# Kernel optimization log

Measured on AMD Instinct MI355X. Metric: run time of the kernel, lower is better.

## Reference

```python
import jax, jax.numpy as jnp
import numpy as np

B, T, C, H = 8, 4096, 384, 64

def setup_inputs() -> dict:
    key = jax.random.key(0)
    k1, k2, k3, k4 = jax.random.split(key, 4)
    x = jax.random.normal(k1, (B, T, C), dtype=jnp.float32)
    Wq = jax.random.normal(k2, (C, H), dtype=jnp.float32) / np.sqrt(C)
    Wk = jax.random.normal(k3, (C, H), dtype=jnp.float32) / np.sqrt(C)
    Wv = jax.random.normal(k4, (C, H), dtype=jnp.float32) / np.sqrt(C)
    return {"x": x, "Wq": Wq, "Wk": Wk, "Wv": Wv}

def reference(x, Wq, Wk, Wv):
    # single-head causal self-attention (dropout in eval mode = identity)
    T_ = x.shape[1]
    q = jnp.einsum('btc,ch->bth', x, Wq)   # [B,T,H]
    k = jnp.einsum('btc,ch->bth', x, Wk)   # [B,T,H]
    v = jnp.einsum('btc,ch->bth', x, Wv)   # [B,T,H]
    scale = 1.0 / jnp.sqrt(jnp.float32(Wq.shape[1]))
    wei = jnp.einsum('bth,bsh->bts', q, k) * scale        # [B,T,T]
    causal = jnp.tril(jnp.ones((T_, T_), dtype=bool))
    wei = jnp.where(causal, wei, -jnp.inf)
    wei = jax.nn.softmax(wei, axis=-1)
    out = jnp.einsum('bts,bsh->bth', wei, v)              # [B,T,H]
    return out
```

## Files before the change

### kernel.cpp

```cpp
#include <hip/hip_runtime.h>
#include <hip/hip_bf16.h>
#include <cstdint>
#include <cstddef>

#define BATCH 8
#define SEQ   4096
#define CDIM  384
#define HDIM  64
#define NSPL  8

typedef __attribute__((ext_vector_type(8)))  __bf16 bf16x8;
typedef __attribute__((ext_vector_type(4)))  float  f32x4;
typedef __attribute__((ext_vector_type(16))) float  f32x16;
typedef __attribute__((ext_vector_type(4)))  short  short4v;

#if __has_builtin(__builtin_amdgcn_permlane32_swap)
#define HAVE_PERMLANE 1
#else
#define HAVE_PERMLANE 0
#endif

typedef __attribute__((address_space(3))) char lds_char;
typedef const __attribute__((address_space(1))) char gbl_char;

static __device__ __forceinline__ void gl_lds16(const void* g, void* l) {
  __builtin_amdgcn_global_load_lds((gbl_char*)g, (lds_char*)l, 16, 0, 0);
}

static __device__ __forceinline__ short f2bf(float f) {
  union { float f; uint32_t u; } v; v.f = f;
  uint32_t r = v.u + 0x7fffu + ((v.u >> 16) & 1u);
  return (short)(r >> 16);
}

static __device__ __forceinline__ float bf2f(short s) {
  union { uint32_t u; float f; } t;
  t.u = ((uint32_t)(uint16_t)s) << 16;
  return t.f;
}

static __device__ __forceinline__ uint32_t cvtpk(float lo, float hi) {
  uint32_t r;
  asm("v_cvt_pk_bf16_f32 %0, %1, %2" : "=v"(r) : "v"(lo), "v"(hi));
  return r;
}

static __device__ __forceinline__ float fexp2(float x) {
  float r;
  asm("v_exp_f32 %0, %1" : "=v"(r) : "v"(x));
  return r;
}

static __device__ __forceinline__ f32x4 mfma16(bf16x8 a, bf16x8 b, f32x4 c) {
  return __builtin_amdgcn_mfma_f32_16x16x32_bf16(a, b, c, 0, 0, 0);
}

static __device__ __forceinline__ f32x16 mfma32(bf16x8 a, bf16x8 b, f32x16 c) {
  return __builtin_amdgcn_mfma_f32_32x32x16_bf16(a, b, c, 0, 0, 0);
}

static __device__ __forceinline__ f32x4 zero4() {
  f32x4 z = {0.f, 0.f, 0.f, 0.f};
  return z;
}

static __device__ __forceinline__ float xhalf(float x, int hi) {
#if HAVE_PERMLANE
  union { float f; uint32_t u; } a; a.f = x;
  auto r = __builtin_amdgcn_permlane32_swap(a.u, a.u, false, false);
  union { uint32_t u; float f; } o; o.u = hi ? r[0] : r[1];
  return o.f;
#else
  return __shfl_xor(x, 32, 64);
#endif
}

static __device__ __forceinline__ void swap32(uint32_t& a, uint32_t& b, int hi) {
#if HAVE_PERMLANE
  auto r = __builtin_amdgcn_permlane32_swap(a, b, false, false);
  a = r[0]; b = r[1];
#else
  uint32_t sa = (uint32_t)__shfl_xor((int)a, 32, 64);
  uint32_t sb = (uint32_t)__shfl_xor((int)b, 32, 64);
  uint32_t na = hi ? sb : a;
  uint32_t nb = hi ? b : sa;
  a = na; b = nb;
#endif
}

static __device__ __forceinline__ float tmax16(const f32x16& v) {
  float a = fmaxf(fmaxf(v[0], v[1]), v[2]);
  float b = fmaxf(fmaxf(v[3], v[4]), v[5]);
  float c = fmaxf(fmaxf(v[6], v[7]), v[8]);
  float d = fmaxf(fmaxf(v[9], v[10]), v[11]);
  float e = fmaxf(fmaxf(v[12], v[13]), v[14]);
  float f = fmaxf(fmaxf(a, b), c);
  float g = fmaxf(fmaxf(d, e), v[15]);
  return fmaxf(f, g);
}

__global__ __launch_bounds__(256) void wpack_kernel(
    const float* __restrict__ Wq, const float* __restrict__ Wk,
    const float* __restrict__ Wv, short* __restrict__ Wt) {
  int idx = blockIdx.x * 256 + threadIdx.x;
  if (idx >= 192 * CDIM) return;
  int n = idx / CDIM;
  int c = idx - n * CDIM;
  int m = n >> 6, h = n & 63;
  const float* W = (m == 0) ? Wq : (m == 1) ? Wk : Wv;
  float s = (m == 0) ? 0.18033688011112042f : 1.0f;
  Wt[idx] = f2bf(W[c * HDIM + h] * s);
}

#define KPAD 136

__global__ __launch_bounds__(256) void qkv_kernel(
    const float* __restrict__ x, const short* __restrict__ Wt,
    short* __restrict__ qb, short* __restrict__ kb, short* __restrict__ vT) {
  __shared__ short xs[2][64][KPAD];
  const int tid = threadIdx.x;
  const int tokbase = blockIdx.x * 64;
  const float4* xg = (const float4*)(x + (size_t)tokbase * CDIM);

  for (int i = tid; i < 2048; i += 256) {
    int r = i >> 5, c4 = i & 31;
    float4 v = xg[r * 96 + c4];
    uint2 st; st.x = cvtpk(v.x, v.y); st.y = cvtpk(v.z, v.w);
    *(uint2*)&xs[0][r][c4 * 4] = st;
  }
  __syncthreads();

  const int wave = tid >> 6;
  const int lane = tid & 63;
  const int l16  = lane & 15;
  const int lq   = lane >> 4;

  f32x4 acc[4][3];
  #pragma unroll
  for (int ai = 0; ai < 4; ++ai)
    #pragma unroll
    for (int j = 0; j < 3; ++j) acc[ai][j] = zero4();

  for (int ch = 0; ch < 3; ++ch) {
    if (ch < 2) {
      const int nb = (ch + 1) & 1;
      for (int i = tid; i < 2048; i += 256) {
        int r = i >> 5, c4 = i & 31;
        float4 v = xg[r * 96 + (ch + 1) * 32 + c4];
        uint2 st; st.x = cvtpk(v.x, v.y); st.y = cvtpk(v.z, v.w);
        *(uint2*)&xs[nb][r][c4 * 4] = st;
      }
    }
    const int cb = ch & 1;
    #pragma unroll
    for (int kk = 0; kk < 4; ++kk) {
      const int k0 = kk * 32;
      bf16x8 a[4];
      #pragma unroll
      for (int ai = 0; ai < 4; ++ai)
        a[ai] = *(const bf16x8*)&xs[cb][ai * 16 + l16][k0 + lq * 8];
      bf16x8 bb[3];
      #pragma unroll
      for (int j = 0; j < 3; ++j) {
        const int nt = wave * 3 + j;
        bb[j] = *(const bf16x8*)&Wt[(size_t)(nt * 16 + l16) * CDIM +
                                    ch * 128 + k0 + lq * 8];
      }
      #pragma unroll
      for (int ai = 0; ai < 4; ++ai)
        #pragma unroll
        for (int j = 0; j < 3; ++j)
          acc[ai][j] = mfma16(a[ai], bb[j], acc[ai][j]);
    }
    __syncthreads();
  }

  const int b     = tokbase >> 12;
  const int tloc0 = tokbase & (SEQ - 1);
  #pragma unroll
  for (int j = 0; j < 3; ++j) {
    const int col = (wave * 3 + j) * 16 + l16;
    const int mat = col >> 6;
    const int h   = col & 63;
    #pragma unroll
    for (int ai = 0; ai < 4; ++ai) {
      const int row0 = ai * 16 + lq * 4;
      if (mat < 2) {
        short* dst = mat ? kb : qb;
        #pragma unroll
        for (int r = 0; r < 4; ++r)
          dst[(size_t)(tokbase + row0 + r) * HDIM + h] = f2bf(acc[ai][j][r]);
      } else {
        union { uint32_t u[2]; short4v s; } sv;
        sv.u[0] = cvtpk(acc[ai][j][0], acc[ai][j][1]);
        sv.u[1] = cvtpk(acc[ai][j][2], acc[ai][j][3]);
        *(short4v*)&vT[(size_t)(b * HDIM + h) * SEQ + (tloc0 + row0)] = sv.s;
      }
    }
  }
}

__global__ __launch_bounds__(256, 3) void attn_kernel(
    const short* __restrict__ qb, const short* __restrict__ kb,
    const short* __restrict__ vT, short* __restrict__ opart,
    float2* __restrict__ mlw) {
  __shared__ short kvbuf[2][2][4096];

  const int tid  = threadIdx.x;
  const int wave = tid >> 6;
  const int lane = tid & 63;
  const int l31  = lane & 31;
  const int hi   = lane >> 5;
  const int bid  = blockIdx.x;
  const int b    = bid & 7;
  const int idx  = bid >> 3;
  const int qt   = 31 - (idx >> 3);
  const int part = idx & 7;
  const int nkv  = 2 * qt + 2;
  const int base = nkv >> 3;
  const int rem  = nkv & 7;
  const int scnt = base + (part < rem ? 1 : 0);
  const int sbeg = part * base + (part < rem ? part : rem);
  const int q0   = qt << 7;
  const int qw0  = q0 + wave * 32;
  const size_t bT = (size_t)b * SEQ;

  const char* kg = (const char*)(kb + bT * HDIM);
  const char* vg = (const char*)(vT + (size_t)b * HDIM * SEQ);

  const int rsub = lane >> 3;
  const int gcol = ((lane & 7) << 4) ^ (rsub << 4);
  const int krb  = wave * 16;

  f32x16 oacc[2];
  #pragma unroll
  for (int hb = 0; hb < 2; ++hb)
    #pragma unroll
    for (int r = 0; r < 16; ++r) oacc[hb][r] = 0.f;
  float m = -1e30f, l = 0.f;

  if (scnt > 0) {
    bf16x8 qf[4];
    {
      const short* qrow = qb + (bT + qw0 + l31) * HDIM + hi * 8;
      #pragma unroll
      for (int t = 0; t < 4; ++t)
        qf[t] = *(const bf16x8*)(qrow + 16 * t);
    }
    const int sw = (l31 & 7) << 4;
    int colk[4];
    #pragma unroll
    for (int t = 0; t < 4; ++t) colk[t] = ((t * 32) + hi * 16) ^ sw;
    const int rbase = l31 * 128;

    {
      const int sf = sbeg << 6;
      #pragma unroll
      for (int i = 0; i < 2; ++i) {
        const int r = krb + i * 8;
        gl_lds16(kg + (size_t)(sf + r + rsub) * 128 + gcol,
                 (char*)&kvbuf[0][0][0] + r * 128);
        gl_lds16(vg + (size_t)(r + rsub) * 8192 + (size_t)sf * 2 + gcol,
                 (char*)&kvbuf[0][1][0] + r * 128);
      }
    }
    __syncthreads();

    int cur = 0;
    for (int it = 0; it < scnt; ++it) {
      const int s0 = (sbeg + it) << 6;
      if (it + 1 < scnt) {
        const int s1 = s0 + 64;
        const int nb = cur ^ 1;
        #pragma unroll
        for (int i = 0; i < 2; ++i) {
          const int r = krb + i * 8;
          gl_lds16(kg + (size_t)(s1 + r + rsub) * 128 + gcol,
                   (char*)&kvbuf[nb][0][0] + r * 128);
          gl_lds16(vg + (size_t)(r + rsub) * 8192 + (size_t)s1 * 2 + gcol,
                   (char*)&kvbuf[nb][1][0] + r * 128);
        }
      }

      if (s0 <= qw0 + 31) {
        const char* bufc = (const char*)kvbuf + cur * 16384;

        f32x16 sacc[2];
        #pragma unroll
        for (int sb = 0; sb < 2; ++sb) {
          #pragma unroll
          for (int r = 0; r < 16; ++r) sacc[sb][r] = 0.f;
          #pragma unroll
          for (int t = 0; t < 4; ++t) {
            bf16x8 kf = *(const bf16x8*)(bufc + sb * 4096 + rbase + colk[t]);
            sacc[sb] = mfma32(kf, qf[t], sacc[sb]);
          }
        }

        if (s0 + 63 > qw0) {
          const int qg = qw0 + l31;
          #pragma unroll
          for (int sb = 0; sb < 2; ++sb)
            #pragma unroll
            for (int r = 0; r < 16; ++r) {
              const int sg = s0 + sb * 32 + (r & 3) + 8 * (r >> 2) + 4 * hi;
              if (sg > qg) sacc[sb][r] = -3e38f;
            }
        }

        float pm = fmaxf(tmax16(sacc[0]), tmax16(sacc[1]));
        pm = fmaxf(pm, xhalf(pm, hi));

        if (!__all(pm <= m + 8.f)) {
          const float mn = fmaxf(m, pm);
          const float sc = fexp2(m - mn);
          m = mn; l *= sc;
          #pragma unroll
          for (int hb = 0; hb < 2; ++hb)
            #pragma unroll
            for (int r = 0; r < 16; ++r) oacc[hb][r] *= sc;
        }

        float p[2][16];
        #pragma unroll
        for (int sb = 0; sb < 2; ++sb)
          #pragma unroll
          for (int r = 0; r < 16; ++r)
            p[sb][r] = fexp2(sacc[sb][r] - m);
        float t8[8];
        #pragma unroll
        for (int sb = 0; sb < 2; ++sb)
          #pragma unroll
          for (int g = 0; g < 4; ++g)
            t8[sb * 4 + g] = (p[sb][4 * g] + p[sb][4 * g + 1]) +
                             (p[sb][4 * g + 2] + p[sb][4 * g + 3]);
        float rs = ((t8[0] + t8[1]) + (t8[2] + t8[3])) +
                   ((t8[4] + t8[5]) + (t8[6] + t8[7]));
        rs += xhalf(rs, hi);
        l += rs;

        uint32_t w[2][4][2];
        #pragma unroll
        for (int sb = 0; sb < 2; ++sb)
          #pragma unroll
          for (int g = 0; g < 4; ++g) {
            w[sb][g][0] = cvtpk(p[sb][4 * g + 0], p[sb][4 * g + 1]);
            w[sb][g][1] = cvtpk(p[sb][4 * g + 2], p[sb][4 * g + 3]);
          }

        bf16x8 pf[4];
        #pragma unroll
        for (int sb = 0; sb < 2; ++sb)
          #pragma unroll
          for (int t = 0; t < 2; ++t) {
            uint32_t a0 = w[sb][2 * t][0], b0 = w[sb][2 * t + 1][0];
            uint32_t a1 = w[sb][2 * t][1], b1 = w[sb][2 * t + 1][1];
            swap32(a0, b0, hi);
            swap32(a1, b1, hi);
            union { uint32_t u[4]; bf16x8 v; } uu;
            uu.u[0] = a0; uu.u[1] = a1; uu.u[2] = b0; uu.u[3] = b1;
            pf[sb * 2 + t] = uu.v;
          }

        __builtin_amdgcn_s_setprio(1);
        #pragma unroll
        for (int hb = 0; hb < 2; ++hb)
          #pragma unroll
          for (int ks = 0; ks < 4; ++ks) {
            bf16x8 vf = *(const bf16x8*)(bufc + 8192 + hb * 4096 + rbase + colk[ks]);
            oacc[hb] = mfma32(vf, pf[ks], oacc[hb]);
          }
        __builtin_amdgcn_s_setprio(0);
      }

      __syncthreads();
      cur ^= 1;
    }
  }

  short* obase = opart + (size_t)part * ((size_t)BATCH * SEQ * HDIM);
  const int q = qw0 + l31;
  #pragma unroll
  for (int hb = 0; hb < 2; ++hb)
    #pragma unroll
    for (int g = 0; g < 4; ++g) {
      uint2 st;
      st.x = cvtpk(oacc[hb][4 * g + 0], oacc[hb][4 * g + 1]);
      st.y = cvtpk(oacc[hb][4 * g + 2], oacc[hb][4 * g + 3]);
      *(uint2*)&obase[(bT + q) * HDIM + hb * 32 + 8 * g + 4 * hi] = st;
    }
  if (lane < 32) {
    float2 ml; ml.x = m; ml.y = l;
    mlw[part * (BATCH * SEQ) + bT + q] = ml;
  }
}

__global__ __launch_bounds__(256) void merge_kernel(
    float* __restrict__ out, const short* __restrict__ opart,
    const float2* __restrict__ mlw) {
  const int g   = blockIdx.x * 256 + threadIdx.x;
  const int row = g >> 4;
  const int c4  = (g & 15) << 2;
  float2 ml[NSPL];
  float mm = -3.4e38f;
  #pragma unroll
  for (int i = 0; i < NSPL; ++i) {
    ml[i] = mlw[i * (BATCH * SEQ) + row];
    mm = fmaxf(mm, ml[i].x);
  }
  float w[NSPL];
  float ls = 0.f;
  #pragma unroll
  for (int i = 0; i < NSPL; ++i) {
    w[i] = fexp2(ml[i].x - mm);
    ls += w[i] * ml[i].y;
  }
  const size_t stride = (size_t)BATCH * SEQ * HDIM;
  const size_t off = (size_t)row * HDIM + c4;
  float a0 = 0.f, a1 = 0.f, a2 = 0.f, a3 = 0.f;
  #pragma unroll
  for (int i = 0; i < NSPL; ++i) {
    short4v s = *(const short4v*)&opart[i * stride + off];
    a0 += w[i] * bf2f(s[0]);
    a1 += w[i] * bf2f(s[1]);
    a2 += w[i] * bf2f(s[2]);
    a3 += w[i] * bf2f(s[3]);
  }
  const float inv = 1.0f / ls;
  float4 r;
  r.x = a0 * inv; r.y = a1 * inv; r.z = a2 * inv; r.w = a3 * inv;
  *(float4*)&out[off] = r;
}

extern "C" void kernel_launch(void* const* d_in, const int* in_sizes, int n_in,
                              void* d_out, int out_size, void* d_ws, size_t ws_size,
                              hipStream_t stream) {
  (void)in_sizes; (void)n_in; (void)out_size; (void)ws_size;
  const float* x  = (const float*)d_in[0];
  const float* Wq = (const float*)d_in[1];
  const float* Wk = (const float*)d_in[2];
  const float* Wv = (const float*)d_in[3];

  const size_t qkvb = (size_t)BATCH * SEQ * HDIM * sizeof(short);
  const size_t opb  = (size_t)NSPL * BATCH * SEQ * HDIM * sizeof(short);
  const size_t mlb  = (size_t)NSPL * BATCH * SEQ * sizeof(float2);
  char* ws = (char*)d_ws;
  short*  qb    = (short*)(ws);
  short*  kb    = (short*)(ws + qkvb);
  short*  vT    = (short*)(ws + 2 * qkvb);
  short*  opart = (short*)(ws + 3 * qkvb);
  float2* mlw   = (float2*)(ws + 3 * qkvb + opb);
  short*  Wt    = (short*)(ws + 3 * qkvb + opb + mlb);

  wpack_kernel<<<dim3((192 * CDIM + 255) / 256), dim3(256), 0, stream>>>(Wq, Wk, Wv, Wt);
  qkv_kernel<<<dim3(BATCH * SEQ / 64), dim3(256), 0, stream>>>(x, Wt, qb, kb, vT);
  attn_kernel<<<dim3(2048), dim3(256), 0, stream>>>(qb, kb, vT, opart, mlw);
  merge_kernel<<<dim3(BATCH * SEQ * HDIM / 4 / 256), dim3(256), 0, stream>>>(
      (float*)d_out, opart, mlw);
}
```

Before: 69.87 us.

## Enlarge attention query tile to 256 rows with 8-wave blocks

Each attention block now uses 512 threads (8 waves) covering a 256-row query tile instead of 128, and the grid is halved. Every K/V tile loaded into LDS is therefore shared by twice as many query rows, which cuts global-to-LDS traffic per query, and each wave issues one load per matrix instead of two. The row-sum cross-half reduction also moves out of the loop to a single exchange at the end. In exchange, blocks are larger and fewer, which can hurt load balance across the causal triangle, and occupancy is capped at 2 blocks per CU.

```diff
diff --git a/kernel.cpp b/kernel.cpp
--- a/kernel.cpp
+++ b/kernel.cpp
@@ -200,7 +200,7 @@
   }
 }
 
-__global__ __launch_bounds__(256, 3) void attn_kernel(
+__global__ __launch_bounds__(512, 2) void attn_kernel(
     const short* __restrict__ qb, const short* __restrict__ kb,
     const short* __restrict__ vT, short* __restrict__ opart,
     float2* __restrict__ mlw) {
@@ -214,14 +214,14 @@
   const int bid  = blockIdx.x;
   const int b    = bid & 7;
   const int idx  = bid >> 3;
-  const int qt   = 31 - (idx >> 3);
+  const int qt   = 15 - (idx >> 3);
   const int part = idx & 7;
-  const int nkv  = 2 * qt + 2;
+  const int nkv  = 4 * qt + 4;
   const int base = nkv >> 3;
   const int rem  = nkv & 7;
   const int scnt = base + (part < rem ? 1 : 0);
   const int sbeg = part * base + (part < rem ? part : rem);
-  const int q0   = qt << 7;
+  const int q0   = qt << 8;
   const int qw0  = q0 + wave * 32;
   const size_t bT = (size_t)b * SEQ;
 
@@ -230,7 +230,7 @@
 
   const int rsub = lane >> 3;
   const int gcol = ((lane & 7) << 4) ^ (rsub << 4);
-  const int krb  = wave * 16;
+  const int krb  = wave * 8;
 
   f32x16 oacc[2];
   #pragma unroll
@@ -255,14 +255,10 @@
 
     {
       const int sf = sbeg << 6;
-      #pragma unroll
-      for (int i = 0; i < 2; ++i) {
-        const int r = krb + i * 8;
-        gl_lds16(kg + (size_t)(sf + r + rsub) * 128 + gcol,
-                 (char*)&kvbuf[0][0][0] + r * 128);
-        gl_lds16(vg + (size_t)(r + rsub) * 8192 + (size_t)sf * 2 + gcol,
-                 (char*)&kvbuf[0][1][0] + r * 128);
-      }
+      gl_lds16(kg + (size_t)(sf + krb + rsub) * 128 + gcol,
+               (char*)&kvbuf[0][0][0] + krb * 128);
+      gl_lds16(vg + (size_t)(krb + rsub) * 8192 + (size_t)sf * 2 + gcol,
+               (char*)&kvbuf[0][1][0] + krb * 128);
     }
     __syncthreads();
 
@@ -272,14 +268,10 @@
       if (it + 1 < scnt) {
         const int s1 = s0 + 64;
         const int nb = cur ^ 1;
-        #pragma unroll
-        for (int i = 0; i < 2; ++i) {
-          const int r = krb + i * 8;
-          gl_lds16(kg + (size_t)(s1 + r + rsub) * 128 + gcol,
-                   (char*)&kvbuf[nb][0][0] + r * 128);
-          gl_lds16(vg + (size_t)(r + rsub) * 8192 + (size_t)s1 * 2 + gcol,
-                   (char*)&kvbuf[nb][1][0] + r * 128);
-        }
+        gl_lds16(kg + (size_t)(s1 + krb + rsub) * 128 + gcol,
+                 (char*)&kvbuf[nb][0][0] + krb * 128);
+        gl_lds16(vg + (size_t)(krb + rsub) * 8192 + (size_t)s1 * 2 + gcol,
+                 (char*)&kvbuf[nb][1][0] + krb * 128);
       }
 
       if (s0 <= qw0 + 31) {
@@ -334,10 +326,8 @@
           for (int g = 0; g < 4; ++g)
             t8[sb * 4 + g] = (p[sb][4 * g] + p[sb][4 * g + 1]) +
                              (p[sb][4 * g + 2] + p[sb][4 * g + 3]);
-        float rs = ((t8[0] + t8[1]) + (t8[2] + t8[3])) +
-                   ((t8[4] + t8[5]) + (t8[6] + t8[7]));
-        rs += xhalf(rs, hi);
-        l += rs;
+        l += ((t8[0] + t8[1]) + (t8[2] + t8[3])) +
+             ((t8[4] + t8[5]) + (t8[6] + t8[7]));
 
         uint32_t w[2][4][2];
         #pragma unroll
@@ -378,6 +368,8 @@
     }
   }
 
+  l += xhalf(l, hi);
+
   short* obase = opart + (size_t)part * ((size_t)BATCH * SEQ * HDIM);
   const int q = qw0 + l31;
   #pragma unroll
@@ -389,7 +381,7 @@
       st.y = cvtpk(oacc[hb][4 * g + 2], oacc[hb][4 * g + 3]);
       *(uint2*)&obase[(bT + q) * HDIM + hb * 32 + 8 * g + 4 * hi] = st;
     }
-  if (lane < 32) {
+  if (hi == 0) {
     float2 ml; ml.x = m; ml.y = l;
     mlw[part * (BATCH * SEQ) + bT + q] = ml;
   }
@@ -454,7 +446,7 @@
 
   wpack_kernel<<<dim3((192 * CDIM + 255) / 256), dim3(256), 0, stream>>>(Wq, Wk, Wv, Wt);
   qkv_kernel<<<dim3(BATCH * SEQ / 64), dim3(256), 0, stream>>>(x, Wt, qb, kb, vT);
-  attn_kernel<<<dim3(2048), dim3(256), 0, stream>>>(qb, kb, vT, opart, mlw);
+  attn_kernel<<<dim3(1024), dim3(512), 0, stream>>>(qb, kb, vT, opart, mlw);
   merge_kernel<<<dim3(BATCH * SEQ * HDIM / 4 / 256), dim3(256), 0, stream>>>(
       (float*)d_out, opart, mlw);
 }
```

After: 69.31 us. Within noise of the previous version (-0.8%).
